# Kernel tuning notes

Measured on AMD Instinct MI355X. Metric: run time of the kernel, lower is better.

Reference implementation:

```python
import jax, jax.numpy as jnp
import numpy as np

D = 1024
H = 16
HD = D // H
FF = 4096
EPS = 1e-5


def setup_inputs() -> dict:
    key = jax.random.key(0)
    ks = jax.random.split(key, 12)
    s = lambda fan_in: 1.0 / np.sqrt(fan_in)
    return {
        "x": jax.random.normal(ks[0], (8, 1024, D), dtype=jnp.float32),
        "ln1_g": jnp.ones((D,), jnp.float32),
        "ln1_b": jnp.zeros((D,), jnp.float32),
        "ln2_g": jnp.ones((D,), jnp.float32),
        "ln2_b": jnp.zeros((D,), jnp.float32),
        "qkv_w": jax.random.uniform(ks[1], (3 * D, D), jnp.float32, -s(D), s(D)),
        "q_bias": jnp.zeros((D,), jnp.float32),
        "v_bias": jnp.zeros((D,), jnp.float32),
        "proj_w": jax.random.uniform(ks[2], (D, D), jnp.float32, -s(D), s(D)),
        "proj_b": jnp.zeros((D,), jnp.float32),
        "fc1_w": jax.random.uniform(ks[3], (FF, D), jnp.float32, -s(D), s(D)),
        "fc1_b": jnp.zeros((FF,), jnp.float32),
        "fc2_w": jax.random.uniform(ks[4], (D, FF), jnp.float32, -s(FF), s(FF)),
        "fc2_b": jnp.zeros((D,), jnp.float32),
    }


def _layernorm(x, g, b):
    mu = jnp.mean(x, axis=-1, keepdims=True)
    var = jnp.mean(jnp.square(x - mu), axis=-1, keepdims=True)
    return (x - mu) * jax.lax.rsqrt(var + EPS) * g + b


def reference(x, ln1_g, ln1_b, ln2_g, ln2_b, qkv_w, q_bias, v_bias,
              proj_w, proj_b, fc1_w, fc1_b, fc2_w, fc2_b):
    b, n, d = x.shape
    scale = HD ** (-0.5)
    # --- attention branch ---
    h = _layernorm(x, ln1_g, ln1_b)
    qkv_bias = jnp.concatenate([q_bias, jnp.zeros_like(v_bias), v_bias])
    qkv = h @ qkv_w.T + qkv_bias  # [b, n, 3d]
    qkv = qkv.reshape(b, n, 3, H, HD).transpose(2, 0, 3, 1, 4)  # [3, b, h, n, hd]
    q, k, v = qkv[0], qkv[1], qkv[2]
    attn = jnp.einsum("bhnd,bhmd->bhnm", q * scale, k)
    attn = jax.nn.softmax(attn, axis=-1)
    o = jnp.einsum("bhnm,bhmd->bhnd", attn, v)
    o = o.transpose(0, 2, 1, 3).reshape(b, n, d)
    x = x + (o @ proj_w.T + proj_b)
    # --- mlp branch ---
    h = _layernorm(x, ln2_g, ln2_b)
    h = jax.nn.gelu(h @ fc1_w.T + fc1_b, approximate=False)
    x = x + (h @ fc2_w.T + fc2_b)
    return x
```

## Files before the change

### kernel.cpp

```cpp
#include <hip/hip_runtime.h>
#include <hip/hip_bf16.h>


typedef __attribute__((ext_vector_type(8))) short short8;
typedef __attribute__((ext_vector_type(4))) float floatx4;

__device__ __forceinline__ unsigned short f2bf(float f) {
  union { __hip_bfloat16 h; unsigned short u; } cv;
  cv.h = __float2bfloat16(f);
  return cv.u;
}

__device__ __forceinline__ float fast_exp2(float x) {
  return __builtin_amdgcn_exp2f(x);
}

__device__ __forceinline__ void async_ld16(const void* g, void* l) {
  __builtin_amdgcn_global_load_lds(
      (const __attribute__((address_space(1))) unsigned int*)g,
      (__attribute__((address_space(3))) unsigned int*)l, 16, 0, 0);
}

__global__ __launch_bounds__(256) void cvt_bf16(const float* __restrict__ in,
                                                unsigned short* __restrict__ out) {
  const long i = ((long)blockIdx.x * 256 + threadIdx.x) * 4;
  const float4 v = *(const float4*)(in + i);
  ushort4 o;
  o.x = f2bf(v.x); o.y = f2bf(v.y); o.z = f2bf(v.z); o.w = f2bf(v.w);
  *(ushort4*)(out + i) = o;
}

__global__ __launch_bounds__(256) void ln_bf16(const float* __restrict__ x,
                                               const float* __restrict__ g,
                                               const float* __restrict__ b,
                                               unsigned short* __restrict__ out) {
  const int row = blockIdx.x;
  const int tid = threadIdx.x;
  const float4 v = ((const float4*)(x + (long)row * 1024))[tid];
  float s = v.x + v.y + v.z + v.w;
  float ss = v.x * v.x + v.y * v.y + v.z * v.z + v.w * v.w;
#pragma unroll
  for (int off = 1; off < 64; off <<= 1) {
    s += __shfl_xor(s, off);
    ss += __shfl_xor(ss, off);
  }
  __shared__ float red[8];
  const int wave = tid >> 6, lane = tid & 63;
  if (lane == 0) { red[wave] = s; red[4 + wave] = ss; }
  __syncthreads();
  if (tid == 0) {
    red[0] = red[0] + red[1] + red[2] + red[3];
    red[4] = red[4] + red[5] + red[6] + red[7];
  }
  __syncthreads();
  const float mu = red[0] * (1.f / 1024.f);
  const float var = red[4] * (1.f / 1024.f) - mu * mu;
  const float rstd = rsqrtf(var + 1e-5f);
  const int c = tid * 4;
  ushort4 o;
  o.x = f2bf((v.x - mu) * rstd * g[c + 0] + b[c + 0]);
  o.y = f2bf((v.y - mu) * rstd * g[c + 1] + b[c + 1]);
  o.z = f2bf((v.z - mu) * rstd * g[c + 2] + b[c + 2]);
  o.w = f2bf((v.w - mu) * rstd * g[c + 3] + b[c + 3]);
  ((ushort4*)(out + (long)row * 1024))[tid] = o;
}

#define BM 128
#define BN 128
#define BK 32

template <int MODE>
__global__ __launch_bounds__(256) void gemm_bt(
    const unsigned short* __restrict__ A, const unsigned short* __restrict__ B,
    int M, int N, int Kd,
    const float* __restrict__ b0, const float* __restrict__ b1,
    const float* __restrict__ resid,
    void* __restrict__ out0, void* __restrict__ out1, void* __restrict__ out2) {
  __shared__ unsigned short lA[2][BM * BK];
  __shared__ unsigned short lB[2][BN * BK];
  const int tid = threadIdx.x;
  const int wave = tid >> 6, lane = tid & 63;
  const int l16 = lane & 15, quad = lane >> 4;
  const int wr = wave >> 1, wc = wave & 1;
  const int bid = blockIdx.x;
  const int xcd = bid & 7;
  const int s = bid >> 3;
  const long m0 = (long)(xcd * 8 + (s & 7)) * BM;
  const long n0 = (long)(s >> 3) * BN;

  const int row = tid >> 2;
  const int kc = (tid & 3) ^ ((row >> 1) & 3);
  const unsigned short* aSrc = A + (m0 + row) * Kd + kc * 8;
  const unsigned short* bSrc = B + (n0 + row) * Kd + kc * 8;
  const int ldsOff0 = wave * 1024;
  const int ldsOff1 = wave * 1024 + 4096;

  floatx4 acc[4][4];
#pragma unroll
  for (int i = 0; i < 4; i++)
#pragma unroll
    for (int j = 0; j < 4; j++) acc[i][j] = (floatx4){0.f, 0.f, 0.f, 0.f};

  async_ld16(aSrc, (char*)&lA[0][0] + ldsOff0);
  async_ld16(aSrc + 64 * Kd, (char*)&lA[0][0] + ldsOff1);
  async_ld16(bSrc, (char*)&lB[0][0] + ldsOff0);
  async_ld16(bSrc + 64 * Kd, (char*)&lB[0][0] + ldsOff1);

  const int sw = ((l16 >> 1) & 3);

  for (int k0 = 0; k0 < Kd; k0 += BK) {
    const int buf = (k0 >> 5) & 1;
    __syncthreads();
    const int kn = k0 + BK;
    if (kn < Kd) {
      async_ld16(aSrc + kn, (char*)&lA[buf ^ 1][0] + ldsOff0);
      async_ld16(aSrc + 64 * Kd + kn, (char*)&lA[buf ^ 1][0] + ldsOff1);
      async_ld16(bSrc + kn, (char*)&lB[buf ^ 1][0] + ldsOff0);
      async_ld16(bSrc + 64 * Kd + kn, (char*)&lB[buf ^ 1][0] + ldsOff1);
    }
    short8 af[4], bfv[4];
#pragma unroll
    for (int mi = 0; mi < 4; mi++) {
      const int r = wr * 64 + mi * 16 + l16;
      af[mi] = *(const short8*)(&lA[buf][(r * 4 + (quad ^ sw)) * 8]);
    }
#pragma unroll
    for (int ni = 0; ni < 4; ni++) {
      const int r = wc * 64 + ni * 16 + l16;
      bfv[ni] = *(const short8*)(&lB[buf][(r * 4 + (quad ^ sw)) * 8]);
    }
#pragma unroll
    for (int mi = 0; mi < 4; mi++)
#pragma unroll
      for (int ni = 0; ni < 4; ni++)
        acc[mi][ni] = __builtin_amdgcn_mfma_f32_16x16x32_bf16(
            af[mi], bfv[ni], acc[mi][ni], 0, 0, 0);
  }

#pragma unroll
  for (int mi = 0; mi < 4; mi++) {
    const long rbase = m0 + wr * 64 + mi * 16 + quad * 4;
#pragma unroll
    for (int ni = 0; ni < 4; ni++) {
      const long cg = n0 + wc * 64 + ni * 16 + l16;
#pragma unroll
      for (int reg = 0; reg < 4; reg++) {
        const long rr = rbase + reg;
        const float val = acc[mi][ni][reg];
        if (MODE == 0) {
          const int which = (int)(cg >> 10);
          const int col = (int)(cg & 1023);
          const int bidx = (int)(rr >> 10), t = (int)(rr & 1023);
          const int head = col >> 6, hd = col & 63;
          const long bh = bidx * 16 + head;
          if (which == 0) {
            ((unsigned short*)out0)[(bh * 1024 + t) * 64 + hd] =
                f2bf((val + b0[col]) * 0.1803368801111244f);
          } else if (which == 1) {
            ((unsigned short*)out1)[(bh * 1024 + t) * 64 + hd] = f2bf(val);
          } else {
            ((unsigned short*)out2)[(bh * 64 + hd) * 1024 + t] =
                f2bf(val + b1[col]);
          }
        } else if (MODE == 1) {
          const long idx = rr * N + cg;
          ((float*)out0)[idx] = resid[idx] + val + b0[cg];
        } else {
          const float u = val + b0[cg];
          const float gl = 0.5f * u * (1.0f + erff(u * 0.70710678118f));
          ((unsigned short*)out0)[rr * N + cg] = f2bf(gl);
        }
      }
    }
  }
}

__global__ __launch_bounds__(256) void attn(const unsigned short* __restrict__ Q,
                                            const unsigned short* __restrict__ Kc,
                                            const unsigned short* __restrict__ Vt,
                                            unsigned short* __restrict__ O) {
  __shared__ unsigned short lK[2][2048];
  __shared__ unsigned short lV[2][2048];
  __shared__ float P[4][2][16][34];
  const int tid = threadIdx.x;
  const int wave = tid >> 6, lane = tid & 63;
  const int l16 = lane & 15, quad = lane >> 4;
  const int bid = blockIdx.x;
  const int xcd = bid & 7;
  const int sl = bid >> 3;
  const int bh = xcd * 16 + (sl & 15);
  const int q0 = (sl >> 4) * 128 + wave * 32;
  const unsigned short* Qb = Q + ((long)bh * 1024 + q0) * 64;
  const unsigned short* Kb = Kc + (long)bh * 65536;
  const unsigned short* Vb = Vt + (long)bh * 65536;

  short8 qf[2][2];
#pragma unroll
  for (int t = 0; t < 2; t++)
#pragma unroll
    for (int h = 0; h < 2; h++)
      qf[t][h] = *(const short8*)(Qb + (t * 16 + l16) * 64 + h * 32 + quad * 8);

  const int kr = tid >> 3;
  const int kc = (tid & 7) ^ (kr & 7);
  const unsigned short* kSrc = Kb + kr * 64 + kc * 8;
  const int vr = tid >> 2;
  const int vc = (tid & 3) ^ (vr & 3) ^ ((vr >> 2) & 3);
  const unsigned short* vSrc = Vb + vr * 1024 + vc * 8;

  floatx4 oacc[2][4];
#pragma unroll
  for (int t = 0; t < 2; t++)
#pragma unroll
    for (int u = 0; u < 4; u++) oacc[t][u] = (floatx4){0.f, 0.f, 0.f, 0.f};
  float lrun[2][4] = {{0.f, 0.f, 0.f, 0.f}, {0.f, 0.f, 0.f, 0.f}};

  async_ld16(kSrc, (char*)&lK[0][0] + wave * 1024);
  async_ld16(vSrc, (char*)&lV[0][0] + wave * 1024);

  const int vca = quad ^ (l16 & 3) ^ ((l16 >> 2) & 3);

  for (int ks = 0; ks < 1024; ks += 32) {
    const int buf = (ks >> 5) & 1;
    __syncthreads();
    const int kn = ks + 32;
    if (kn < 1024) {
      async_ld16(kSrc + kn * 64, (char*)&lK[buf ^ 1][0] + wave * 1024);
      async_ld16(vSrc + kn,      (char*)&lV[buf ^ 1][0] + wave * 1024);
    }
    short8 kf[2][2];
#pragma unroll
    for (int i = 0; i < 2; i++)
#pragma unroll
      for (int h = 0; h < 2; h++) {
        const int gr = (i * 16 + l16) * 8 + ((h * 4 + quad) ^ (l16 & 7));
        kf[i][h] = *(const short8*)(&lK[buf][gr * 8]);
      }
    floatx4 s[2][2];
#pragma unroll
    for (int t = 0; t < 2; t++)
#pragma unroll
      for (int i = 0; i < 2; i++) {
        const floatx4 z = {0.f, 0.f, 0.f, 0.f};
        floatx4 a = __builtin_amdgcn_mfma_f32_16x16x32_bf16(qf[t][0], kf[i][0], z, 0, 0, 0);
        s[t][i] = __builtin_amdgcn_mfma_f32_16x16x32_bf16(qf[t][1], kf[i][1], a, 0, 0, 0);
      }
#pragma unroll
    for (int t = 0; t < 2; t++)
#pragma unroll
      for (int r = 0; r < 4; r++) {
        const float p0 = fast_exp2(s[t][0][r]);
        const float p1 = fast_exp2(s[t][1][r]);
        lrun[t][r] += p0 + p1;
        P[wave][t][quad * 4 + r][l16] = p0;
        P[wave][t][quad * 4 + r][16 + l16] = p1;
      }
    short8 vf[4];
#pragma unroll
    for (int u = 0; u < 4; u++)
      vf[u] = *(const short8*)(&lV[buf][((u * 16 + l16) * 4 + vca) * 8]);
    short8 pf[2];
#pragma unroll
    for (int t = 0; t < 2; t++) {
      const float* pr = &P[wave][t][l16][quad * 8];
      const floatx4 pa = *(const floatx4*)pr;
      const floatx4 pb = *(const floatx4*)(pr + 4);
      pf[t][0] = (short)f2bf(pa[0]); pf[t][1] = (short)f2bf(pa[1]);
      pf[t][2] = (short)f2bf(pa[2]); pf[t][3] = (short)f2bf(pa[3]);
      pf[t][4] = (short)f2bf(pb[0]); pf[t][5] = (short)f2bf(pb[1]);
      pf[t][6] = (short)f2bf(pb[2]); pf[t][7] = (short)f2bf(pb[3]);
    }
#pragma unroll
    for (int t = 0; t < 2; t++)
#pragma unroll
      for (int u = 0; u < 4; u++)
        oacc[t][u] = __builtin_amdgcn_mfma_f32_16x16x32_bf16(pf[t], vf[u], oacc[t][u], 0, 0, 0);
  }

  const int b = bh >> 4, h = bh & 15;
#pragma unroll
  for (int t = 0; t < 2; t++) {
#pragma unroll
    for (int r = 0; r < 4; r++) {
      float lr = lrun[t][r];
      lr += __shfl_xor(lr, 1);
      lr += __shfl_xor(lr, 2);
      lr += __shfl_xor(lr, 4);
      lr += __shfl_xor(lr, 8);
      const float linv = 1.0f / lr;
#pragma unroll
      for (int u = 0; u < 4; u++) {
        O[((long)b * 1024 + q0 + t * 16 + quad * 4 + r) * 1024 + h * 64 + u * 16 + l16] =
            f2bf(oacc[t][u][r] * linv);
      }
    }
  }
}

extern "C" void kernel_launch(void* const* d_in, const int* in_sizes, int n_in,
                              void* d_out, int out_size, void* d_ws, size_t ws_size,
                              hipStream_t stream) {
  const float* x      = (const float*)d_in[0];
  const float* ln1_g  = (const float*)d_in[1];
  const float* ln1_b  = (const float*)d_in[2];
  const float* ln2_g  = (const float*)d_in[3];
  const float* ln2_b  = (const float*)d_in[4];
  const float* qkv_w  = (const float*)d_in[5];
  const float* q_bias = (const float*)d_in[6];
  const float* v_bias = (const float*)d_in[7];
  const float* proj_w = (const float*)d_in[8];
  const float* proj_b = (const float*)d_in[9];
  const float* fc1_w  = (const float*)d_in[10];
  const float* fc1_b  = (const float*)d_in[11];
  const float* fc2_w  = (const float*)d_in[12];
  const float* fc2_b  = (const float*)d_in[13];
  float* out = (float*)d_out;

  char* ws = (char*)d_ws;
  unsigned short* Wqkv  = (unsigned short*)(ws);
  unsigned short* Wproj = (unsigned short*)(ws + 6291456);
  unsigned short* Wfc1  = (unsigned short*)(ws + 8388608);
  unsigned short* Wfc2  = (unsigned short*)(ws + 16777216);
  float*          X1    = (float*)        (ws + 25165824);
  unsigned short* Hbuf  = (unsigned short*)(ws + 58720256);
  unsigned short* Qbuf  = (unsigned short*)(ws + 75497472);
  unsigned short* Kbuf  = (unsigned short*)(ws + 92274688);
  unsigned short* Vtbuf = (unsigned short*)(ws + 109051904);
  unsigned short* Obuf  = (unsigned short*)(ws + 125829120);
  unsigned short* ACT   = Qbuf;

  cvt_bf16<<<3072 * 1024 / 1024, 256, 0, stream>>>(qkv_w, Wqkv);
  cvt_bf16<<<1024 * 1024 / 1024, 256, 0, stream>>>(proj_w, Wproj);
  cvt_bf16<<<4096 * 1024 / 1024, 256, 0, stream>>>(fc1_w, Wfc1);
  cvt_bf16<<<4096 * 1024 / 1024, 256, 0, stream>>>(fc2_w, Wfc2);

  ln_bf16<<<8192, 256, 0, stream>>>(x, ln1_g, ln1_b, Hbuf);
  gemm_bt<0><<<24 * 64, 256, 0, stream>>>(Hbuf, Wqkv, 8192, 3072, 1024,
                                          q_bias, v_bias, nullptr,
                                          Qbuf, Kbuf, Vtbuf);
  attn<<<1024, 256, 0, stream>>>(Qbuf, Kbuf, Vtbuf, Obuf);
  gemm_bt<1><<<8 * 64, 256, 0, stream>>>(Obuf, Wproj, 8192, 1024, 1024,
                                         proj_b, nullptr, x,
                                         X1, nullptr, nullptr);
  ln_bf16<<<8192, 256, 0, stream>>>(X1, ln2_g, ln2_b, Hbuf);
  gemm_bt<2><<<32 * 64, 256, 0, stream>>>(Hbuf, Wfc1, 8192, 4096, 1024,
                                          fc1_b, nullptr, nullptr,
                                          ACT, nullptr, nullptr);
  gemm_bt<1><<<8 * 64, 256, 0, stream>>>(ACT, Wfc2, 8192, 1024, 4096,
                                         fc2_b, nullptr, X1,
                                         out, nullptr, nullptr);
  (void)in_sizes; (void)n_in; (void)out_size; (void)ws_size;
}
```

Measured before the change: 586.1 us.

## Add 256x256-tile 8-wave GEMM with phased LDS pipelining for QKV and FC1

Adds a new GEMM kernel that uses 512 threads and 256x256 output tiles with double-buffered async global-to-LDS loads. The K loop is split into four MFMA phases, each interleaved with staged loads, explicit vmcnt waits, barriers and raised wave priority. The QKV and FC1 projections now use this kernel, which aims for more data reuse per LDS load and better overlap of memory traffic with MFMA work. In exchange, the per-block register and LDS footprint is larger and the grids are smaller (384 and 512 blocks), which can leave compute units underused or cause tail effects.

Measured after the change: 602.3 us. +2.8%, slower.

```diff
diff --git a/kernel.cpp b/kernel.cpp
--- a/kernel.cpp
+++ b/kernel.cpp
@@ -20,6 +20,8 @@
       (const __attribute__((address_space(1))) unsigned int*)g,
       (__attribute__((address_space(3))) unsigned int*)l, 16, 0, 0);
 }
+
+#define VMCNT(n) asm volatile("s_waitcnt vmcnt(" #n ")" ::: "memory")
 
 __global__ __launch_bounds__(256) void cvt_bf16(const float* __restrict__ in,
                                                 unsigned short* __restrict__ out) {
@@ -175,6 +177,161 @@
   }
 }
 
+template <int MODE>
+__global__ __launch_bounds__(512, 2) void gemm8(
+    const unsigned short* __restrict__ A, const unsigned short* __restrict__ B,
+    int M, int N, int Kd,
+    const float* __restrict__ b0, const float* __restrict__ b1,
+    const float* __restrict__ resid,
+    void* __restrict__ out0, void* __restrict__ out1, void* __restrict__ out2) {
+  __shared__ __align__(16) unsigned short lds[2][8][4096];
+  const int tid = threadIdx.x;
+  const int wave = tid >> 6, lane = tid & 63;
+  const int l16 = lane & 15, quad = lane >> 4;
+  const int q7 = l16 & 7;
+  const int wr = wave >> 2, wc = wave & 3;
+  const int bid = blockIdx.x;
+  const int xcd = bid & 7, s = bid >> 3;
+  const long m0 = (long)(xcd * 4 + (s & 3)) * 256;
+  const long n0 = (long)(s >> 2) * 256;
+  const int NT = Kd >> 6;
+
+  const int srow = tid >> 3;
+  const int sg = (tid & 7) ^ (srow & 7);
+  const unsigned short* aS = A + (m0 + srow) * Kd + sg * 8;
+  const unsigned short* bS = B + (n0 + srow) * Kd + sg * 8;
+  const int wvOff = wave * 1024;
+
+#define STAGE_A(c, kk, bp) \
+  async_ld16(aS + (long)(c) * 64 * Kd + (kk), (char*)&lds[bp][c][0] + wvOff)
+#define STAGE_B(c, kk, bp) \
+  async_ld16(bS + (long)(c) * 64 * Kd + (kk), (char*)&lds[bp][4 + (c)][0] + wvOff)
+
+  floatx4 acc[8][4];
+#pragma unroll
+  for (int i = 0; i < 8; i++)
+#pragma unroll
+    for (int j = 0; j < 4; j++) acc[i][j] = (floatx4){0.f, 0.f, 0.f, 0.f};
+
+  short8 af[4][2];
+  short8 bf[4][2];
+
+#define RD_A(CP)                                                     \
+  _Pragma("unroll") for (int mi = 0; mi < 4; mi++) {                 \
+    const char* p_ = (CP) + (mi * 16 + l16) * 128;                   \
+    af[mi][0] = *(const short8*)(p_ + ((quad ^ q7) * 16));           \
+    af[mi][1] = *(const short8*)(p_ + (((4 + quad) ^ q7) * 16));     \
+  }
+#define RD_B(HN)                                                         \
+  _Pragma("unroll") for (int ni = 0; ni < 2; ni++) {                     \
+    const char* p_ = bC + (((HN)*32) + ni * 16 + l16) * 128;             \
+    bf[(HN)*2 + ni][0] = *(const short8*)(p_ + ((quad ^ q7) * 16));      \
+    bf[(HN)*2 + ni][1] = *(const short8*)(p_ + (((4 + quad) ^ q7) * 16)); \
+  }
+#define MFMA_PHASE(HM, HN)                                                   \
+  __builtin_amdgcn_s_setprio(1);                                             \
+  _Pragma("unroll") for (int mi = 0; mi < 4; mi++) {                         \
+    _Pragma("unroll") for (int ni = 0; ni < 2; ni++) {                       \
+      floatx4 c_ = acc[(HM)*4 + mi][(HN)*2 + ni];                            \
+      c_ = __builtin_amdgcn_mfma_f32_16x16x32_bf16(af[mi][0],                \
+                                                   bf[(HN)*2 + ni][0], c_,   \
+                                                   0, 0, 0);                 \
+      c_ = __builtin_amdgcn_mfma_f32_16x16x32_bf16(af[mi][1],                \
+                                                   bf[(HN)*2 + ni][1], c_,   \
+                                                   0, 0, 0);                 \
+      acc[(HM)*4 + mi][(HN)*2 + ni] = c_;                                    \
+    }                                                                        \
+  }                                                                          \
+  __builtin_amdgcn_s_setprio(0);
+
+  STAGE_A(0, 0, 0); STAGE_A(2, 0, 0);
+  STAGE_B(0, 0, 0); STAGE_B(1, 0, 0); STAGE_B(2, 0, 0); STAGE_B(3, 0, 0);
+  STAGE_A(0, 64, 1); STAGE_A(2, 64, 1);
+  STAGE_A(1, 0, 0); STAGE_A(3, 0, 0);
+  VMCNT(4);
+  __builtin_amdgcn_s_barrier();
+
+  for (int u = 0; u < NT; ++u) {
+    const int buf = u & 1, nxt = buf ^ 1;
+    const long kk1 = (long)(u + 1) << 6;
+    const long kk2 = (long)(u + 2) << 6;
+    const char* aC0 = (const char*)&lds[buf][wr * 2][0];
+    const char* aC1 = (const char*)&lds[buf][wr * 2 + 1][0];
+    const char* bC = (const char*)&lds[buf][4 + wc][0];
+
+    RD_A(aC0);
+    RD_B(0);
+    if (u + 1 < NT) { STAGE_B(0, kk1, nxt); STAGE_B(1, kk1, nxt); }
+    __builtin_amdgcn_s_barrier();
+    MFMA_PHASE(0, 0);
+    __builtin_amdgcn_s_barrier();
+
+    RD_B(1);
+    if (u + 1 < NT) { STAGE_B(2, kk1, nxt); STAGE_B(3, kk1, nxt); }
+    __builtin_amdgcn_s_barrier();
+    MFMA_PHASE(0, 1);
+    if (u + 1 < NT) { VMCNT(4); } else { VMCNT(0); }
+    __builtin_amdgcn_s_barrier();
+
+    RD_A(aC1);
+    if (u + 2 < NT) { STAGE_A(0, kk2, buf); STAGE_A(2, kk2, buf); }
+    __builtin_amdgcn_s_barrier();
+    MFMA_PHASE(1, 1);
+    __builtin_amdgcn_s_barrier();
+
+    if (u + 1 < NT) { STAGE_A(1, kk1, nxt); STAGE_A(3, kk1, nxt); }
+    __builtin_amdgcn_s_barrier();
+    MFMA_PHASE(1, 0);
+    if (u < NT - 1) {
+      if (u + 2 < NT) { VMCNT(4); } else { VMCNT(2); }
+      __builtin_amdgcn_s_barrier();
+    }
+  }
+
+#pragma unroll
+  for (int mi2 = 0; mi2 < 8; mi2++) {
+    const long rbase = m0 + wr * 128 + mi2 * 16 + quad * 4;
+#pragma unroll
+    for (int nj = 0; nj < 4; nj++) {
+      const long cg = n0 + wc * 64 + nj * 16 + l16;
+#pragma unroll
+      for (int reg = 0; reg < 4; reg++) {
+        const long rr = rbase + reg;
+        const float val = acc[mi2][nj][reg];
+        if (MODE == 0) {
+          const int which = (int)(cg >> 10);
+          const int col = (int)(cg & 1023);
+          const int bidx = (int)(rr >> 10), t = (int)(rr & 1023);
+          const int head = col >> 6, hd = col & 63;
+          const long bh = bidx * 16 + head;
+          if (which == 0) {
+            ((unsigned short*)out0)[(bh * 1024 + t) * 64 + hd] =
+                f2bf((val + b0[col]) * 0.1803368801111244f);
+          } else if (which == 1) {
+            ((unsigned short*)out1)[(bh * 1024 + t) * 64 + hd] = f2bf(val);
+          } else {
+            ((unsigned short*)out2)[(bh * 64 + hd) * 1024 + t] =
+                f2bf(val + b1[col]);
+          }
+        } else if (MODE == 1) {
+          const long idx = rr * N + cg;
+          ((float*)out0)[idx] = resid[idx] + val + b0[cg];
+        } else {
+          const float u2 = val + b0[cg];
+          const float gl = 0.5f * u2 * (1.0f + erff(u2 * 0.70710678118f));
+          ((unsigned short*)out0)[rr * N + cg] = f2bf(gl);
+        }
+      }
+    }
+  }
+  (void)M;
+#undef STAGE_A
+#undef STAGE_B
+#undef RD_A
+#undef RD_B
+#undef MFMA_PHASE
+}
+
 __global__ __launch_bounds__(256) void attn(const unsigned short* __restrict__ Q,
                                             const unsigned short* __restrict__ Kc,
                                             const unsigned short* __restrict__ Vt,
@@ -236,21 +393,21 @@
         const int gr = (i * 16 + l16) * 8 + ((h * 4 + quad) ^ (l16 & 7));
         kf[i][h] = *(const short8*)(&lK[buf][gr * 8]);
       }
-    floatx4 s[2][2];
+    floatx4 sres[2][2];
 #pragma unroll
     for (int t = 0; t < 2; t++)
 #pragma unroll
       for (int i = 0; i < 2; i++) {
         const floatx4 z = {0.f, 0.f, 0.f, 0.f};
         floatx4 a = __builtin_amdgcn_mfma_f32_16x16x32_bf16(qf[t][0], kf[i][0], z, 0, 0, 0);
-        s[t][i] = __builtin_amdgcn_mfma_f32_16x16x32_bf16(qf[t][1], kf[i][1], a, 0, 0, 0);
+        sres[t][i] = __builtin_amdgcn_mfma_f32_16x16x32_bf16(qf[t][1], kf[i][1], a, 0, 0, 0);
       }
 #pragma unroll
     for (int t = 0; t < 2; t++)
 #pragma unroll
       for (int r = 0; r < 4; r++) {
-        const float p0 = fast_exp2(s[t][0][r]);
-        const float p1 = fast_exp2(s[t][1][r]);
+        const float p0 = fast_exp2(sres[t][0][r]);
+        const float p1 = fast_exp2(sres[t][1][r]);
         lrun[t][r] += p0 + p1;
         P[wave][t][quad * 4 + r][l16] = p0;
         P[wave][t][quad * 4 + r][16 + l16] = p1;
@@ -335,17 +492,17 @@
   cvt_bf16<<<4096 * 1024 / 1024, 256, 0, stream>>>(fc2_w, Wfc2);
 
   ln_bf16<<<8192, 256, 0, stream>>>(x, ln1_g, ln1_b, Hbuf);
-  gemm_bt<0><<<24 * 64, 256, 0, stream>>>(Hbuf, Wqkv, 8192, 3072, 1024,
-                                          q_bias, v_bias, nullptr,
-                                          Qbuf, Kbuf, Vtbuf);
+  gemm8<0><<<384, 512, 0, stream>>>(Hbuf, Wqkv, 8192, 3072, 1024,
+                                    q_bias, v_bias, nullptr,
+                                    Qbuf, Kbuf, Vtbuf);
   attn<<<1024, 256, 0, stream>>>(Qbuf, Kbuf, Vtbuf, Obuf);
   gemm_bt<1><<<8 * 64, 256, 0, stream>>>(Obuf, Wproj, 8192, 1024, 1024,
                                          proj_b, nullptr, x,
                                          X1, nullptr, nullptr);
   ln_bf16<<<8192, 256, 0, stream>>>(X1, ln2_g, ln2_b, Hbuf);
-  gemm_bt<2><<<32 * 64, 256, 0, stream>>>(Hbuf, Wfc1, 8192, 4096, 1024,
-                                          fc1_b, nullptr, nullptr,
-                                          ACT, nullptr, nullptr);
+  gemm8<2><<<512, 512, 0, stream>>>(Hbuf, Wfc1, 8192, 4096, 1024,
+                                    fc1_b, nullptr, nullptr,
+                                    ACT, nullptr, nullptr);
   gemm_bt<1><<<8 * 64, 256, 0, stream>>>(ACT, Wfc2, 8192, 1024, 4096,
                                          fc2_b, nullptr, X1,
                                          out, nullptr, nullptr);
```

## Triple-buffer GEMM LDS loads with explicit vmcnt waits, vectorize V-transpose stores

Applied to the files above, without the earlier changes.

The GEMM main loop moves from double to triple buffering in LDS. Loads are issued two K-steps ahead, and explicit s_waitcnt vmcnt plus a raw s_barrier replace __syncthreads, so global-to-LDS copies overlap more MFMA work. In the QKV epilogue, the transposed V output is now written as packed 4-element ushort4 stores instead of scalar stores. The extra buffer raises LDS use per block, which may reduce occupancy. A local variable in the attention kernel is also renamed.

Result: faster. 557.2 us (-4.9%).

```diff
diff --git a/kernel.cpp b/kernel.cpp
--- a/kernel.cpp
+++ b/kernel.cpp
@@ -20,6 +20,8 @@
       (const __attribute__((address_space(1))) unsigned int*)g,
       (__attribute__((address_space(3))) unsigned int*)l, 16, 0, 0);
 }
+
+#define VMCNT(n) asm volatile("s_waitcnt vmcnt(" #n ")" ::: "memory")
 
 __global__ __launch_bounds__(256) void cvt_bf16(const float* __restrict__ in,
                                                 unsigned short* __restrict__ out) {
@@ -67,7 +69,6 @@
 
 #define BM 128
 #define BN 128
-#define BK 32
 
 template <int MODE>
 __global__ __launch_bounds__(256) void gemm_bt(
@@ -76,8 +77,8 @@
     const float* __restrict__ b0, const float* __restrict__ b1,
     const float* __restrict__ resid,
     void* __restrict__ out0, void* __restrict__ out1, void* __restrict__ out2) {
-  __shared__ unsigned short lA[2][BM * BK];
-  __shared__ unsigned short lB[2][BN * BK];
+  __shared__ unsigned short lA[3][BM * 32];
+  __shared__ unsigned short lB[3][BN * 32];
   const int tid = threadIdx.x;
   const int wave = tid >> 6, lane = tid & 63;
   const int l16 = lane & 15, quad = lane >> 4;
@@ -101,22 +102,30 @@
 #pragma unroll
     for (int j = 0; j < 4; j++) acc[i][j] = (floatx4){0.f, 0.f, 0.f, 0.f};
 
-  async_ld16(aSrc, (char*)&lA[0][0] + ldsOff0);
-  async_ld16(aSrc + 64 * Kd, (char*)&lA[0][0] + ldsOff1);
-  async_ld16(bSrc, (char*)&lB[0][0] + ldsOff0);
-  async_ld16(bSrc + 64 * Kd, (char*)&lB[0][0] + ldsOff1);
+#pragma unroll
+  for (int bp = 0; bp < 2; bp++) {
+    const int kk = bp * 32;
+    async_ld16(aSrc + kk, (char*)&lA[bp][0] + ldsOff0);
+    async_ld16(aSrc + 64 * Kd + kk, (char*)&lA[bp][0] + ldsOff1);
+    async_ld16(bSrc + kk, (char*)&lB[bp][0] + ldsOff0);
+    async_ld16(bSrc + 64 * Kd + kk, (char*)&lB[bp][0] + ldsOff1);
+  }
 
   const int sw = ((l16 >> 1) & 3);
 
-  for (int k0 = 0; k0 < Kd; k0 += BK) {
-    const int buf = (k0 >> 5) & 1;
-    __syncthreads();
-    const int kn = k0 + BK;
+  int buf = 0;
+  for (int k0 = 0; k0 < Kd; k0 += 32) {
+    if (k0 + 32 < Kd) { VMCNT(4); } else { VMCNT(0); }
+    __builtin_amdgcn_sched_barrier(0);
+    __builtin_amdgcn_s_barrier();
+    __builtin_amdgcn_sched_barrier(0);
+    const int kn = k0 + 64;
     if (kn < Kd) {
-      async_ld16(aSrc + kn, (char*)&lA[buf ^ 1][0] + ldsOff0);
-      async_ld16(aSrc + 64 * Kd + kn, (char*)&lA[buf ^ 1][0] + ldsOff1);
-      async_ld16(bSrc + kn, (char*)&lB[buf ^ 1][0] + ldsOff0);
-      async_ld16(bSrc + 64 * Kd + kn, (char*)&lB[buf ^ 1][0] + ldsOff1);
+      const int bp = (buf + 2 >= 3) ? buf - 1 : buf + 2;
+      async_ld16(aSrc + kn, (char*)&lA[bp][0] + ldsOff0);
+      async_ld16(aSrc + 64 * Kd + kn, (char*)&lA[bp][0] + ldsOff1);
+      async_ld16(bSrc + kn, (char*)&lB[bp][0] + ldsOff0);
+      async_ld16(bSrc + 64 * Kd + kn, (char*)&lB[bp][0] + ldsOff1);
     }
     short8 af[4], bfv[4];
 #pragma unroll
@@ -135,6 +144,7 @@
       for (int ni = 0; ni < 4; ni++)
         acc[mi][ni] = __builtin_amdgcn_mfma_f32_16x16x32_bf16(
             af[mi], bfv[ni], acc[mi][ni], 0, 0, 0);
+    buf = (buf + 1 >= 3) ? 0 : buf + 1;
   }
 
 #pragma unroll
@@ -143,36 +153,54 @@
 #pragma unroll
     for (int ni = 0; ni < 4; ni++) {
       const long cg = n0 + wc * 64 + ni * 16 + l16;
-#pragma unroll
-      for (int reg = 0; reg < 4; reg++) {
-        const long rr = rbase + reg;
-        const float val = acc[mi][ni][reg];
-        if (MODE == 0) {
-          const int which = (int)(cg >> 10);
-          const int col = (int)(cg & 1023);
-          const int bidx = (int)(rr >> 10), t = (int)(rr & 1023);
-          const int head = col >> 6, hd = col & 63;
+      if (MODE == 0) {
+        const int which = (int)(cg >> 10);
+        const int col = (int)(cg & 1023);
+        const int head = col >> 6, hd = col & 63;
+        if (which == 2) {
+          const int bidx = (int)(rbase >> 10);
+          const int t = (int)(rbase & 1023);
           const long bh = bidx * 16 + head;
-          if (which == 0) {
-            ((unsigned short*)out0)[(bh * 1024 + t) * 64 + hd] =
-                f2bf((val + b0[col]) * 0.1803368801111244f);
-          } else if (which == 1) {
-            ((unsigned short*)out1)[(bh * 1024 + t) * 64 + hd] = f2bf(val);
+          const float bv = b1[col];
+          ushort4 pk;
+          pk.x = f2bf(acc[mi][ni][0] + bv);
+          pk.y = f2bf(acc[mi][ni][1] + bv);
+          pk.z = f2bf(acc[mi][ni][2] + bv);
+          pk.w = f2bf(acc[mi][ni][3] + bv);
+          *(ushort4*)((unsigned short*)out2 + (bh * 64 + hd) * 1024 + t) = pk;
+        } else {
+#pragma unroll
+          for (int reg = 0; reg < 4; reg++) {
+            const long rr = rbase + reg;
+            const float val = acc[mi][ni][reg];
+            const int bidx = (int)(rr >> 10), t = (int)(rr & 1023);
+            const long bh = bidx * 16 + head;
+            if (which == 0) {
+              ((unsigned short*)out0)[(bh * 1024 + t) * 64 + hd] =
+                  f2bf((val + b0[col]) * 0.1803368801111244f);
+            } else {
+              ((unsigned short*)out1)[(bh * 1024 + t) * 64 + hd] = f2bf(val);
+            }
+          }
+        }
+      } else {
+#pragma unroll
+        for (int reg = 0; reg < 4; reg++) {
+          const long rr = rbase + reg;
+          const float val = acc[mi][ni][reg];
+          if (MODE == 1) {
+            const long idx = rr * N + cg;
+            ((float*)out0)[idx] = resid[idx] + val + b0[cg];
           } else {
-            ((unsigned short*)out2)[(bh * 64 + hd) * 1024 + t] =
-                f2bf(val + b1[col]);
+            const float u = val + b0[cg];
+            const float gl = 0.5f * u * (1.0f + erff(u * 0.70710678118f));
+            ((unsigned short*)out0)[rr * N + cg] = f2bf(gl);
           }
-        } else if (MODE == 1) {
-          const long idx = rr * N + cg;
-          ((float*)out0)[idx] = resid[idx] + val + b0[cg];
-        } else {
-          const float u = val + b0[cg];
-          const float gl = 0.5f * u * (1.0f + erff(u * 0.70710678118f));
-          ((unsigned short*)out0)[rr * N + cg] = f2bf(gl);
         }
       }
     }
   }
+  (void)M;
 }
 
 __global__ __launch_bounds__(256) void attn(const unsigned short* __restrict__ Q,
@@ -236,21 +264,21 @@
         const int gr = (i * 16 + l16) * 8 + ((h * 4 + quad) ^ (l16 & 7));
         kf[i][h] = *(const short8*)(&lK[buf][gr * 8]);
       }
-    floatx4 s[2][2];
+    floatx4 sres[2][2];
 #pragma unroll
     for (int t = 0; t < 2; t++)
 #pragma unroll
       for (int i = 0; i < 2; i++) {
         const floatx4 z = {0.f, 0.f, 0.f, 0.f};
         floatx4 a = __builtin_amdgcn_mfma_f32_16x16x32_bf16(qf[t][0], kf[i][0], z, 0, 0, 0);
-        s[t][i] = __builtin_amdgcn_mfma_f32_16x16x32_bf16(qf[t][1], kf[i][1], a, 0, 0, 0);
+        sres[t][i] = __builtin_amdgcn_mfma_f32_16x16x32_bf16(qf[t][1], kf[i][1], a, 0, 0, 0);
       }
 #pragma unroll
     for (int t = 0; t < 2; t++)
 #pragma unroll
       for (int r = 0; r < 4; r++) {
-        const float p0 = fast_exp2(s[t][0][r]);
-        const float p1 = fast_exp2(s[t][1][r]);
+        const float p0 = fast_exp2(sres[t][0][r]);
+        const float p1 = fast_exp2(sres[t][1][r]);
         lrun[t][r] += p0 + p1;
         P[wave][t][quad * 4 + r][l16] = p0;
         P[wave][t][quad * 4 + r][16 + l16] = p1;
```
